# Optimization experiments

Measured on AMD Instinct MI355X. Metric: run time of the kernel, lower is better.

The kernel has to match this reference:

```python
import jax, jax.numpy as jnp
import numpy as np
from jax import lax

DN = ('NHWC', 'HWIO', 'NHWC')
COMMIT = 0.25  # commitment_cost


def _conv(x, w, b, s):
    return lax.conv_general_dilated(x, w, (s, s), 'SAME', dimension_numbers=DN) + b


def _convT(x, w, b, s):
    return lax.conv_transpose(x, w, (s, s), 'SAME', dimension_numbers=DN) + b


def setup_inputs() -> dict:
    key = jax.random.key(0)
    ks = jax.random.split(key, 12)
    B, H, W = 128, 128, 128
    D, K = 64, 512  # embedding_dim, num_embeddings

    def wp(k, shape):
        fan_in = shape[0] * shape[1] * shape[2]
        return (jax.random.normal(k, shape, jnp.float32) / np.sqrt(fan_in)).astype(jnp.float32)

    return {
        'x': jax.random.uniform(ks[0], (B, H, W, 3), jnp.float32),
        'enc_w1': wp(ks[1], (4, 4, 3, 32)),   'enc_b1': jnp.zeros((32,), jnp.float32),
        'enc_w2': wp(ks[2], (4, 4, 32, 64)),  'enc_b2': jnp.zeros((64,), jnp.float32),
        'enc_w3': wp(ks[3], (4, 4, 64, 128)), 'enc_b3': jnp.zeros((128,), jnp.float32),
        'enc_w4': wp(ks[4], (2, 2, 128, D)),  'enc_b4': jnp.zeros((D,), jnp.float32),
        'emb': jax.random.normal(ks[5], (K, D), jnp.float32),
        'dec_w1': wp(ks[6], (2, 2, D, 128)),  'dec_b1': jnp.zeros((128,), jnp.float32),
        'dec_w2': wp(ks[7], (4, 4, 128, 64)), 'dec_b2': jnp.zeros((64,), jnp.float32),
        'dec_w3': wp(ks[8], (4, 4, 64, 32)),  'dec_b3': jnp.zeros((32,), jnp.float32),
        'dec_w4': wp(ks[9], (4, 4, 32, 3)),   'dec_b4': jnp.zeros((3,), jnp.float32),
    }


def _forward(x, enc_w1, enc_b1, enc_w2, enc_b2, enc_w3, enc_b3, enc_w4, enc_b4,
             emb, dec_w1, dec_b1, dec_w2, dec_b2, dec_w3, dec_b3, dec_w4, dec_b4):
    # ---- encoder: 128 -> 64 -> 32 -> 16 (SAME, stride 2) -> 16 (stride 1) ----
    z = jax.nn.relu(_conv(x, enc_w1, enc_b1, 2))
    z = jax.nn.relu(_conv(z, enc_w2, enc_b2, 2))
    z = jax.nn.relu(_conv(z, enc_w3, enc_b3, 2))
    z = _conv(z, enc_w4, enc_b4, 1)                     # [B, 16, 16, D]

    # ---- vector quantizer ----
    B, D = z.shape[0], emb.shape[1]
    flat = z.reshape(B, -1, D)                          # [B, N, D]
    d2 = (jnp.sum(flat * flat, axis=2, keepdims=True)
          - 2.0 * jnp.einsum('bnd,kd->bnk', flat, emb)
          + jnp.sum(emb * emb, axis=1))                 # [B, N, K]
    idx = jnp.argmin(d2, axis=2)                        # [B, N] int
    q = emb[idx].reshape(z.shape)                       # gather == one_hot @ emb
    loss = COMMIT * jnp.mean((lax.stop_gradient(q) - z) ** 2)
    q_st = z + lax.stop_gradient(q - z)                 # straight-through

    # ---- decoder: 16 -> 16 (stride 1) -> 32 -> 64 -> 128 ----
    y = jax.nn.relu(_convT(q_st, dec_w1, dec_b1, 1))
    y = jax.nn.relu(_convT(y, dec_w2, dec_b2, 2))
    y = jax.nn.relu(_convT(y, dec_w3, dec_b3, 2))
    y = jax.nn.sigmoid(_convT(y, dec_w4, dec_b4, 2))    # [B, 128, 128, 3]
    return y, loss, idx


def reference(x, enc_w1, enc_b1, enc_w2, enc_b2, enc_w3, enc_b3, enc_w4, enc_b4,
              emb, dec_w1, dec_b1, dec_w2, dec_b2, dec_w3, dec_b3, dec_w4, dec_b4):
    return _forward(x, enc_w1, enc_b1, enc_w2, enc_b2, enc_w3, enc_b3, enc_w4, enc_b4,
                    emb, dec_w1, dec_b1, dec_w2, dec_b2, dec_w3, dec_b3, dec_w4, dec_b4)
```

## Files before the change

kernel.cpp:

```cpp
#include <hip/hip_runtime.h>
#include <hip/hip_bf16.h>

typedef __bf16 bf16x8_t __attribute__((ext_vector_type(8)));
typedef float  f32x4_t  __attribute__((ext_vector_type(4)));

__device__ inline bf16x8_t ld_bf16x8(const __hip_bfloat16* p) {
    return *reinterpret_cast<const bf16x8_t*>(p);
}
__device__ inline bf16x8_t zero_bf16x8() {
    bf16x8_t z;
#pragma unroll
    for (int i = 0; i < 8; ++i) z[i] = (__bf16)0.0f;
    return z;
}

__device__ inline void split3f(float v, __bf16& h, __bf16& m, __bf16& l) {
    unsigned u;  __builtin_memcpy(&u, &v, 4);
    unsigned uh = u & 0xffff0000u;
    float fh;    __builtin_memcpy(&fh, &uh, 4);
    float r = v - fh;
    unsigned ur; __builtin_memcpy(&ur, &r, 4);
    unsigned um = ur & 0xffff0000u;
    float fm;    __builtin_memcpy(&fm, &um, 4);
    float r2 = r - fm;
    unsigned ul; __builtin_memcpy(&ul, &r2, 4);
    unsigned short hs = (unsigned short)(uh >> 16);
    unsigned short ms = (unsigned short)(um >> 16);
    unsigned short ls = (unsigned short)(ul >> 16);
    __builtin_memcpy(&h, &hs, 2);
    __builtin_memcpy(&m, &ms, 2);
    __builtin_memcpy(&l, &ls, 2);
}

__global__ __launch_bounds__(256) void enc1_kernel(
    const float* __restrict__ x, const float* __restrict__ w,
    const float* __restrict__ bias, float* __restrict__ y)
{
    __shared__ float xs[34*66*3];
    __shared__ float wsm[1536];

    const int n  = blockIdx.x >> 3;
    const int th = (blockIdx.x >> 1) & 3;
    const int tw = blockIdx.x & 1;
    const int HO0 = th*16, WO0 = tw*32;
    const int HI0 = 2*HO0 - 1, WI0 = 2*WO0 - 1;
    const int t = threadIdx.x;

    for (int i = t; i < 1536; i += 256) wsm[i] = w[i];
    for (int i = t; i < 34*66*3; i += 256) {
        int row = i / 198; int j = i - row*198;
        int wi_l = j / 3;  int c = j - wi_l*3;
        int hi = HI0 + row, wi = WI0 + wi_l;
        float v = 0.0f;
        if (hi >= 0 && hi < 128 && wi >= 0 && wi < 128)
            v = x[((n*128 + hi)*128 + wi)*3 + c];
        xs[i] = v;
    }
    __syncthreads();

    const int wl = t & 15, hl = t >> 4;
    float acc0[32], acc1[32];
#pragma unroll
    for (int f4 = 0; f4 < 8; ++f4) {
        float4 bv = *(const float4*)(bias + 4*f4);
        acc0[4*f4+0]=bv.x; acc0[4*f4+1]=bv.y; acc0[4*f4+2]=bv.z; acc0[4*f4+3]=bv.w;
        acc1[4*f4+0]=bv.x; acc1[4*f4+1]=bv.y; acc1[4*f4+2]=bv.z; acc1[4*f4+3]=bv.w;
    }
    for (int r = 0; r < 4; ++r) {
#pragma unroll
        for (int s = 0; s < 4; ++s) {
#pragma unroll
            for (int c = 0; c < 3; ++c) {
                float xv0 = xs[(2*hl + r)*198 + (2*wl + s)*3 + c];
                float xv1 = xs[(2*hl + r)*198 + (2*(wl+16) + s)*3 + c];
                const float* wp = wsm + ((r*4 + s)*3 + c)*32;
#pragma unroll
                for (int f4 = 0; f4 < 8; ++f4) {
                    float4 wv = *(const float4*)(wp + 4*f4);
                    acc0[4*f4+0] = fmaf(xv0, wv.x, acc0[4*f4+0]);
                    acc0[4*f4+1] = fmaf(xv0, wv.y, acc0[4*f4+1]);
                    acc0[4*f4+2] = fmaf(xv0, wv.z, acc0[4*f4+2]);
                    acc0[4*f4+3] = fmaf(xv0, wv.w, acc0[4*f4+3]);
                    acc1[4*f4+0] = fmaf(xv1, wv.x, acc1[4*f4+0]);
                    acc1[4*f4+1] = fmaf(xv1, wv.y, acc1[4*f4+1]);
                    acc1[4*f4+2] = fmaf(xv1, wv.z, acc1[4*f4+2]);
                    acc1[4*f4+3] = fmaf(xv1, wv.w, acc1[4*f4+3]);
                }
            }
        }
    }
    float* y0 = y + ((size_t)((n*64 + HO0 + hl)*64) + WO0 + wl)*32;
#pragma unroll
    for (int f4 = 0; f4 < 8; ++f4) {
        float4 o0 = make_float4(fmaxf(acc0[4*f4+0],0.f), fmaxf(acc0[4*f4+1],0.f),
                                fmaxf(acc0[4*f4+2],0.f), fmaxf(acc0[4*f4+3],0.f));
        *(float4*)(y0 + 4*f4) = o0;
    }
    float* y1 = y0 + 16*32;
#pragma unroll
    for (int f4 = 0; f4 < 8; ++f4) {
        float4 o1 = make_float4(fmaxf(acc1[4*f4+0],0.f), fmaxf(acc1[4*f4+1],0.f),
                                fmaxf(acc1[4*f4+2],0.f), fmaxf(acc1[4*f4+3],0.f));
        *(float4*)(y1 + 4*f4) = o1;
    }
}

__global__ void prep_wpk(const float* __restrict__ w, __hip_bfloat16* __restrict__ out,
                         int TAPS, int CIN, int COUT)
{
    const int NF = COUT >> 4, KC = CIN >> 5;
    int total = TAPS*3*NF*KC*512;
    int i = blockIdx.x*256 + threadIdx.x;
    if (i >= total) return;
    int tmp = i;
    int j = tmp & 7;      tmp >>= 3;
    int lane = tmp & 63;  tmp >>= 6;
    int kc = tmp % KC;    tmp /= KC;
    int nf = tmp % NF;    tmp /= NF;
    int plane = tmp % 3;  int tap = tmp / 3;
    int l15 = lane & 15, quad = lane >> 4;
    int f = nf*16 + l15;
    int c = kc*32 + quad*8 + j;
    float v = w[(tap*CIN + c)*COUT + f];
    __bf16 h, m, l;
    split3f(v, h, m, l);
    ((__bf16*)out)[i] = (plane == 0) ? h : (plane == 1) ? m : l;
}

__global__ void prep_wdk(const float* __restrict__ w, __hip_bfloat16* __restrict__ out,
                         int TAPS, int CIN, int COUT)
{
    const int NF = COUT >> 4, KC = CIN >> 5;
    int total = TAPS*NF*KC*512;
    int i = blockIdx.x*256 + threadIdx.x;
    if (i >= total) return;
    int tmp = i;
    int j = tmp & 7;      tmp >>= 3;
    int lane = tmp & 63;  tmp >>= 6;
    int kc = tmp % KC;    tmp /= KC;
    int nf = tmp % NF;    tmp /= NF;
    int tap = tmp;
    int l15 = lane & 15, quad = lane >> 4;
    int f = nf*16 + l15;
    int c = kc*32 + quad*8 + j;
    out[i] = __float2bfloat16(w[(tap*CIN + c)*COUT + f]);
}

__global__ void prep_wb4(const float* __restrict__ w, __hip_bfloat16* __restrict__ out)
{
    int i = blockIdx.x*256 + threadIdx.x;
    if (i >= 16*64*8) return;
    int j = i & 7;
    int lane = (i >> 3) & 63;
    int g = i >> 9;
    int f = lane & 15;
    int c = (lane >> 4)*8 + j;
    float v = (f < 3) ? w[g*96 + c*3 + f] : 0.0f;
    out[i] = __float2bfloat16(v);
}

__global__ void prep_wek(const float* __restrict__ emb, __hip_bfloat16* __restrict__ out)
{
    int i = blockIdx.x*256 + threadIdx.x;
    if (i >= 32*2*3*512) return;
    int tmp = i;
    int j = tmp & 7;      tmp >>= 3;
    int lane = tmp & 63;  tmp >>= 6;
    int plane = tmp % 3;  tmp /= 3;
    int kc = tmp & 1;     int nf = tmp >> 1;
    int code = nf*16 + (lane & 15);
    int c = kc*32 + (lane >> 4)*8 + j;
    float v = emb[code*64 + c];
    __bf16 h, m, l;
    split3f(v, h, m, l);
    ((__bf16*)out)[i] = (plane == 0) ? h : (plane == 1) ? m : l;
}

__global__ void prep_se(const float* __restrict__ emb, float* __restrict__ se)
{
    int k = blockIdx.x*256 + threadIdx.x;
    if (k >= 512) return;
    float s = 0.0f;
    for (int d = 0; d < 64; ++d) {
        float e = emb[k*64 + d];
        s = fmaf(e, e, s);
    }
    se[k] = s;
}

template<int R,int S,int CIN,int COUT,int IWL,int OWL,int STR,int PAD,int ACT,int INF32,int OUTF32,int NSPLIT>
__global__ __launch_bounds__(256) void mfma_encB(
    const void* __restrict__ xin,
    const __hip_bfloat16* __restrict__ wpk,
    const float* __restrict__ bias,
    __hip_bfloat16* __restrict__ yout,
    float* __restrict__ yf)
{
    constexpr int IW = 1 << IWL, OW = 1 << OWL;
    constexpr int NF = COUT / 16, KC = CIN / 32, TAPS = R*S;
    constexpr int NFB = NF / NSPLIT;
    constexpr int PIECE = NFB*KC*64;
    constexpr int CHUNK8 = 3*PIECE;
    __shared__ bf16x8_t ldsB[CHUNK8];

    const int nf0 = (int)blockIdx.y * NFB;
    const int t = threadIdx.x;
    const int wave = t >> 6, lane = t & 63;
    const int l15 = lane & 15, quad = lane >> 4;

    const int m  = blockIdx.x*64 + wave*16 + l15;
    const int wp_ = m & (OW-1);
    const int hp_ = (m >> OWL) & (OW-1);
    const int np_ = m >> (2*OWL);

    f32x4_t acc[NFB];
#pragma unroll
    for (int nf = 0; nf < NFB; ++nf) {
        float bv = bias[(nf0 + nf)*16 + l15];
        acc[nf][0] = bv; acc[nf][1] = bv; acc[nf][2] = bv; acc[nf][3] = bv;
    }
    const bf16x8_t zv = zero_bf16x8();

    for (int tap = 0; tap < TAPS; ++tap) {
        __syncthreads();
        {
            const bf16x8_t* base = (const bf16x8_t*)wpk + (size_t)tap*(3*NF*KC*64);
            for (int i8 = t; i8 < CHUNK8; i8 += 256) {
                int plane = i8 / PIECE;
                int rem = i8 - plane*PIECE;
                ldsB[i8] = base[(size_t)(plane*NF + nf0)*KC*64 + rem];
            }
        }
        __syncthreads();

        const int r = tap / S, s = tap % S;
        const int hi = hp_*STR - PAD + r;
        const int wi = wp_*STR - PAD + s;
        const bool v = (hi >= 0) && (hi < IW) && (wi >= 0) && (wi < IW);
        const int hic = v ? hi : 0, wic = v ? wi : 0;
        const size_t pix = (size_t)(np_*IW + hic)*IW + wic;

#pragma unroll
        for (int kc = 0; kc < KC; ++kc) {
            bf16x8_t ah, am_, al_;
            if (INF32) {
                const float* af = (const float*)xin + pix*CIN + kc*32 + quad*8;
                float xv[8];
                if (v) {
                    *(float4*)(xv+0) = *(const float4*)(af);
                    *(float4*)(xv+4) = *(const float4*)(af + 4);
                } else {
#pragma unroll
                    for (int jj = 0; jj < 8; ++jj) xv[jj] = 0.0f;
                }
#pragma unroll
                for (int jj = 0; jj < 8; ++jj) {
                    __bf16 th, tm, tl;
                    split3f(xv[jj], th, tm, tl);
                    ah[jj] = th; am_[jj] = tm; al_[jj] = tl;
                }
            } else {
                const __hip_bfloat16* ap = (const __hip_bfloat16*)xin
                    + pix*(3*CIN) + kc*32 + quad*8;
                ah  = v ? ld_bf16x8(ap)           : zv;
                am_ = v ? ld_bf16x8(ap + CIN)     : zv;
                al_ = v ? ld_bf16x8(ap + 2*CIN)   : zv;
            }
#pragma unroll
            for (int nf = 0; nf < NFB; ++nf) {
                bf16x8_t bh = ldsB[(0*NFB + nf)*KC*64 + kc*64 + lane];
                bf16x8_t bm = ldsB[(1*NFB + nf)*KC*64 + kc*64 + lane];
                bf16x8_t bl = ldsB[(2*NFB + nf)*KC*64 + kc*64 + lane];
                acc[nf] = __builtin_amdgcn_mfma_f32_16x16x32_bf16(al_, bh, acc[nf], 0, 0, 0);
                acc[nf] = __builtin_amdgcn_mfma_f32_16x16x32_bf16(ah,  bl, acc[nf], 0, 0, 0);
                acc[nf] = __builtin_amdgcn_mfma_f32_16x16x32_bf16(am_, bm, acc[nf], 0, 0, 0);
                acc[nf] = __builtin_amdgcn_mfma_f32_16x16x32_bf16(am_, bh, acc[nf], 0, 0, 0);
                acc[nf] = __builtin_amdgcn_mfma_f32_16x16x32_bf16(ah,  bm, acc[nf], 0, 0, 0);
                acc[nf] = __builtin_amdgcn_mfma_f32_16x16x32_bf16(ah,  bh, acc[nf], 0, 0, 0);
            }
        }
    }

#pragma unroll
    for (int nf = 0; nf < NFB; ++nf) {
#pragma unroll
        for (int i = 0; i < 4; ++i) {
            int mo = blockIdx.x*64 + wave*16 + quad*4 + i;
            int wo = mo & (OW-1), ho = (mo >> OWL) & (OW-1), no = mo >> (2*OWL);
            size_t opix = (size_t)(no*OW + ho)*OW + wo;
            float vv = acc[nf][i];
            if (ACT) vv = fmaxf(vv, 0.0f);
            if (OUTF32) {
                yf[opix*COUT + (nf0 + nf)*16 + l15] = vv;
            } else {
                __bf16 h, mm2, l;
                split3f(vv, h, mm2, l);
                __bf16* yb = (__bf16*)yout + opix*(3*COUT) + (nf0 + nf)*16 + l15;
                yb[0]        = h;
                yb[COUT]     = mm2;
                yb[2*COUT]   = l;
            }
        }
    }
}

template<int CIN,int COUT,int SWL,int CONVT,int NSPLIT>
__global__ __launch_bounds__(256) void mfma_decB(
    const __hip_bfloat16* __restrict__ xin,
    const __hip_bfloat16* __restrict__ wdk,
    const float* __restrict__ bias,
    __hip_bfloat16* __restrict__ yout)
{
    constexpr int SW = 1 << SWL;
    constexpr int NF = COUT / 16, KC = CIN / 32;
    constexpr int NFB = NF / NSPLIT;
    constexpr int CHUNK8 = NFB*KC*64;
    __shared__ bf16x8_t ldsB[CHUNK8];

    const int ph = CONVT ? (int)(blockIdx.y >> 1) : 0;
    const int pw = CONVT ? (int)(blockIdx.y & 1) : 0;
    const int nf0 = (CONVT ? (int)blockIdx.z : (int)blockIdx.y) * NFB;
    const int t = threadIdx.x;
    const int wave = t >> 6, lane = t & 63;
    const int l15 = lane & 15, quad = lane >> 4;

    const int m  = blockIdx.x*64 + wave*16 + l15;
    const int wp_ = m & (SW-1);
    const int hp_ = (m >> SWL) & (SW-1);
    const int np_ = m >> (2*SWL);

    f32x4_t acc[NFB];
#pragma unroll
    for (int nf = 0; nf < NFB; ++nf) {
        float bv = bias[(nf0 + nf)*16 + l15];
        acc[nf][0] = bv; acc[nf][1] = bv; acc[nf][2] = bv; acc[nf][3] = bv;
    }
    const bf16x8_t zv = zero_bf16x8();

    for (int tap = 0; tap < 4; ++tap) {
        const int rr = tap >> 1, ss = tap & 1;
        const int widx = CONVT ? ((ph + 2*rr)*4 + (pw + 2*ss)) : tap;
        __syncthreads();
        {
            const bf16x8_t* base = (const bf16x8_t*)wdk
                + (size_t)widx*(NF*KC*64) + (size_t)nf0*KC*64;
            for (int i8 = t; i8 < CHUNK8; i8 += 256) ldsB[i8] = base[i8];
        }
        __syncthreads();

        const int hi = hp_ + ph - 1 + rr;
        const int wi = wp_ + pw - 1 + ss;
        const bool v = (hi >= 0) && (hi < SW) && (wi >= 0) && (wi < SW);
        const int hic = v ? hi : 0, wic = v ? wi : 0;
        const __hip_bfloat16* ap = xin + (size_t)((np_*SW + hic)*SW + wic)*CIN + quad*8;
#pragma unroll
        for (int kc = 0; kc < KC; ++kc) {
            bf16x8_t a = v ? ld_bf16x8(ap + kc*32) : zv;
#pragma unroll
            for (int nf = 0; nf < NFB; ++nf) {
                bf16x8_t b = ldsB[(nf*KC + kc)*64 + lane];
                acc[nf] = __builtin_amdgcn_mfma_f32_16x16x32_bf16(a, b, acc[nf], 0, 0, 0);
            }
        }
    }

    constexpr int HOUT = CONVT ? 2*SW : SW;
#pragma unroll
    for (int nf = 0; nf < NFB; ++nf) {
#pragma unroll
        for (int i = 0; i < 4; ++i) {
            int mo = blockIdx.x*64 + wave*16 + quad*4 + i;
            int wo = mo & (SW-1), ho = (mo >> SWL) & (SW-1), no = mo >> (2*SWL);
            int hoo = CONVT ? 2*ho + ph : ho;
            int woo = CONVT ? 2*wo + pw : wo;
            float vv = fmaxf(acc[nf][i], 0.0f);
            yout[((size_t)(no*HOUT + hoo)*HOUT + woo)*COUT + (nf0 + nf)*16 + l15] = __float2bfloat16(vv);
        }
    }
}

__global__ __launch_bounds__(256) void dec4_mfma(
    const __hip_bfloat16* __restrict__ x, const __hip_bfloat16* __restrict__ wb,
    const float* __restrict__ bias, float* __restrict__ y)
{
    __shared__ __hip_bfloat16 xs[6*66*40];

    const int n  = blockIdx.x >> 4;
    const int R0 = (blockIdx.x & 15) * 4;
    const int t  = threadIdx.x;
    const int wave = t >> 6, lane = t & 63;
    const int l15 = lane & 15, quad = lane >> 4;

    bf16x8_t wreg[16];
#pragma unroll
    for (int g = 0; g < 16; ++g)
        wreg[g] = ld_bf16x8(wb + (size_t)(g*64 + lane)*8);

    const float bv = (l15 < 3) ? bias[l15] : 0.0f;

    for (int slot = t; slot < 6*66*4; slot += 256) {
        int row = slot / 264;
        int rem = slot - row*264;
        int col = rem >> 2, c8 = rem & 3;
        int xi = R0 - 1 + row, xc = col - 1;
        uint4 val = make_uint4(0u,0u,0u,0u);
        if (xi >= 0 && xi < 64 && xc >= 0 && xc < 64)
            val = *(const uint4*)(x + ((size_t)((n*64 + xi)*64) + xc)*32 + c8*8);
        *(uint4*)(xs + (row*66 + col)*40 + c8*8) = val;
    }
    __syncthreads();

    for (int r4 = 0; r4 < 4; ++r4) {
        bf16x8_t af[3][3];
#pragma unroll
        for (int dr = 0; dr < 3; ++dr)
#pragma unroll
            for (int dc = 0; dc < 3; ++dc)
                af[dr][dc] = *(const bf16x8_t*)(xs
                    + ((r4 + dr)*66 + (wave*16 + l15 + dc))*40 + quad*8);

#pragma unroll
        for (int ph = 0; ph < 2; ++ph)
#pragma unroll
        for (int pw = 0; pw < 2; ++pw) {
            f32x4_t acc;
            acc[0] = bv; acc[1] = bv; acc[2] = bv; acc[3] = bv;
#pragma unroll
            for (int rr = 0; rr < 2; ++rr)
#pragma unroll
            for (int ss = 0; ss < 2; ++ss) {
                const int g = (ph + 2*rr)*4 + (pw + 2*ss);
                acc = __builtin_amdgcn_mfma_f32_16x16x32_bf16(
                          af[ph+rr][pw+ss], wreg[g], acc, 0, 0, 0);
            }
            if (l15 < 3) {
#pragma unroll
                for (int i = 0; i < 4; ++i) {
                    int pc = wave*16 + quad*4 + i;
                    int ho = 2*(R0 + r4) + ph, wo = 2*pc + pw;
                    float vv = 1.0f / (1.0f + __expf(-acc[i]));
                    y[((size_t)(n*128 + ho)*128 + wo)*3 + l15] = vv;
                }
            }
        }
    }
}

__global__ void zero_loss(float* p) {
    if (threadIdx.x == 0 && blockIdx.x == 0) *p = 0.0f;
}

__global__ __launch_bounds__(256) void vq_mfma(
    const float* __restrict__ z, const __hip_bfloat16* __restrict__ wek,
    const float* __restrict__ se, const float* __restrict__ emb,
    __hip_bfloat16* __restrict__ qb, float* __restrict__ idx_out,
    float* __restrict__ loss_out, float loss_scale)
{
    __shared__ float ses[512];
    __shared__ float rv[64*16];
    __shared__ int   ri[64*16];
    __shared__ int   mi[64];
    __shared__ float lred[256];

    const int t = threadIdx.x;
    const int wave = t >> 6, lane = t & 63;
    const int l15 = lane & 15, quad = lane >> 4;
    const int pos0 = blockIdx.x * 64;

    for (int i = t; i < 512; i += 256) ses[i] = se[i];

    const int prow = pos0 + wave*16 + l15;
    bf16x8_t ah[2], am[2], al[2];
#pragma unroll
    for (int kc = 0; kc < 2; ++kc) {
        float xv[8];
        *(float4*)(xv+0) = *(const float4*)(z + (size_t)prow*64 + kc*32 + quad*8);
        *(float4*)(xv+4) = *(const float4*)(z + (size_t)prow*64 + kc*32 + quad*8 + 4);
#pragma unroll
        for (int jj = 0; jj < 8; ++jj) {
            __bf16 th, tm, tl;
            split3f(xv[jj], th, tm, tl);
            ah[kc][jj] = th; am[kc][jj] = tm; al[kc][jj] = tl;
        }
    }

    f32x4_t acc[32];
#pragma unroll
    for (int nf = 0; nf < 32; ++nf) {
        acc[nf][0] = 0.f; acc[nf][1] = 0.f; acc[nf][2] = 0.f; acc[nf][3] = 0.f;
    }

#pragma unroll 8
    for (int nf = 0; nf < 32; ++nf) {
#pragma unroll
        for (int kc = 0; kc < 2; ++kc) {
            const bf16x8_t* bp = (const bf16x8_t*)wek + (size_t)((nf*2 + kc)*3)*64 + lane;
            bf16x8_t bh = bp[0];
            bf16x8_t bm = bp[64];
            bf16x8_t bl = bp[128];
            acc[nf] = __builtin_amdgcn_mfma_f32_16x16x32_bf16(al[kc], bh, acc[nf], 0, 0, 0);
            acc[nf] = __builtin_amdgcn_mfma_f32_16x16x32_bf16(ah[kc], bl, acc[nf], 0, 0, 0);
            acc[nf] = __builtin_amdgcn_mfma_f32_16x16x32_bf16(am[kc], bm, acc[nf], 0, 0, 0);
            acc[nf] = __builtin_amdgcn_mfma_f32_16x16x32_bf16(am[kc], bh, acc[nf], 0, 0, 0);
            acc[nf] = __builtin_amdgcn_mfma_f32_16x16x32_bf16(ah[kc], bm, acc[nf], 0, 0, 0);
            acc[nf] = __builtin_amdgcn_mfma_f32_16x16x32_bf16(ah[kc], bh, acc[nf], 0, 0, 0);
        }
    }
    __syncthreads();

    float best[4]; int bidx[4];
#pragma unroll
    for (int i = 0; i < 4; ++i) { best[i] = 3.4e38f; bidx[i] = 0; }
#pragma unroll
    for (int nf = 0; nf < 32; ++nf) {
        const int code = nf*16 + l15;
        const float seC = ses[code];
#pragma unroll
        for (int i = 0; i < 4; ++i) {
            float d = fmaf(-2.0f, acc[nf][i], seC);
            if (d < best[i]) { best[i] = d; bidx[i] = code; }
        }
    }
#pragma unroll
    for (int i = 0; i < 4; ++i) {
        int p = wave*16 + quad*4 + i;
        rv[p*16 + l15] = best[i];
        ri[p*16 + l15] = bidx[i];
    }
    __syncthreads();
    if (t < 64) {
        float bd = rv[t*16]; int bi = ri[t*16];
#pragma unroll
        for (int k = 1; k < 16; ++k) {
            float v = rv[t*16 + k]; int id = ri[t*16 + k];
            if (v < bd || (v == bd && id < bi)) { bd = v; bi = id; }
        }
        mi[t] = bi;
        idx_out[pos0 + t] = (float)bi;
    }
    __syncthreads();

    float part = 0.0f;
    for (int j = t; j < 4096; j += 256) {
        int p = j >> 6, d = j & 63;
        float ev = emb[(size_t)mi[p]*64 + d];
        float zz = z[(size_t)(pos0 + p)*64 + d];
        float df = ev - zz;
        part = fmaf(df, df, part);
        qb[(size_t)pos0*64 + j] = __float2bfloat16(ev);
    }
    lred[t] = part;
    __syncthreads();
    for (int s = 128; s > 0; s >>= 1) {
        if (t < s) lred[t] += lred[t + s];
        __syncthreads();
    }
    if (t == 0) atomicAdd(loss_out, lred[0] * loss_scale);
}

extern "C" void kernel_launch(void* const* d_in, const int* in_sizes, int n_in,
                              void* d_out, int out_size, void* d_ws, size_t ws_size,
                              hipStream_t stream)
{
    const float* x   = (const float*)d_in[0];
    const float* ew1 = (const float*)d_in[1];  const float* eb1 = (const float*)d_in[2];
    const float* ew2 = (const float*)d_in[3];  const float* eb2 = (const float*)d_in[4];
    const float* ew3 = (const float*)d_in[5];  const float* eb3 = (const float*)d_in[6];
    const float* ew4 = (const float*)d_in[7];  const float* eb4 = (const float*)d_in[8];
    const float* emb = (const float*)d_in[9];
    const float* dw1 = (const float*)d_in[10]; const float* db1 = (const float*)d_in[11];
    const float* dw2 = (const float*)d_in[12]; const float* db2 = (const float*)d_in[13];
    const float* dw3 = (const float*)d_in[14]; const float* db3 = (const float*)d_in[15];
    const float* dw4 = (const float*)d_in[16]; const float* db4 = (const float*)d_in[17];

    float* outy = (float*)d_out;
    float* outl = outy + 6291456;
    float* outi = outl + 1;

    char* W = (char*)d_ws;
    float*          e1  = (float*)         (W + 0);
    __hip_bfloat16* e2p = (__hip_bfloat16*)(W + 67108864);
    __hip_bfloat16* e3p = (__hip_bfloat16*)(W + 0);
    float*          z   = (float*)         (W + 25165824);
    __hip_bfloat16* qb  = (__hip_bfloat16*)(W + 33554432);
    __hip_bfloat16* d1o = (__hip_bfloat16*)(W + 37748736);
    __hip_bfloat16* d2o = (__hip_bfloat16*)(W + 46137344);
    __hip_bfloat16* d3o = (__hip_bfloat16*)(W + 67108864);
    __hip_bfloat16* wp2 = (__hip_bfloat16*)(W + 117440512);
    __hip_bfloat16* wp3 = wp2 + 98304;
    __hip_bfloat16* wp4 = wp3 + 393216;
    __hip_bfloat16* wd1 = wp4 + 98304;
    __hip_bfloat16* wd2 = wd1 + 32768;
    __hip_bfloat16* wd3 = wd2 + 131072;
    __hip_bfloat16* wb4 = wd3 + 32768;
    __hip_bfloat16* wek = wb4 + 8192;
    float*          seb = (float*)(wek + 98304);

    hipLaunchKernelGGL(prep_wpk, dim3(384),  dim3(256), 0, stream, ew2, wp2, 16, 32, 64);
    hipLaunchKernelGGL(prep_wpk, dim3(1536), dim3(256), 0, stream, ew3, wp3, 16, 64, 128);
    hipLaunchKernelGGL(prep_wpk, dim3(384),  dim3(256), 0, stream, ew4, wp4, 4, 128, 64);
    hipLaunchKernelGGL(prep_wdk, dim3(128),  dim3(256), 0, stream, dw1, wd1, 4, 64, 128);
    hipLaunchKernelGGL(prep_wdk, dim3(512),  dim3(256), 0, stream, dw2, wd2, 16, 128, 64);
    hipLaunchKernelGGL(prep_wdk, dim3(128),  dim3(256), 0, stream, dw3, wd3, 16, 64, 32);
    hipLaunchKernelGGL(prep_wb4, dim3(32),   dim3(256), 0, stream, dw4, wb4);
    hipLaunchKernelGGL(prep_wek, dim3(384),  dim3(256), 0, stream, emb, wek);
    hipLaunchKernelGGL(prep_se,  dim3(2),    dim3(256), 0, stream, emb, seb);

    hipLaunchKernelGGL(enc1_kernel, dim3(1024), dim3(256), 0, stream, x, ew1, eb1, e1);
    hipLaunchKernelGGL((mfma_encB<4,4,32,64,6,5,2,1,1,1,0,1>), dim3(2048), dim3(256), 0, stream,
                       (const void*)e1, wp2, eb2, e2p, (float*)nullptr);
    hipLaunchKernelGGL((mfma_encB<4,4,64,128,5,4,2,1,1,0,0,2>), dim3(512,2), dim3(256), 0, stream,
                       (const void*)e2p, wp3, eb3, e3p, (float*)nullptr);
    hipLaunchKernelGGL((mfma_encB<2,2,128,64,4,4,1,0,0,0,1,2>), dim3(512,2), dim3(256), 0, stream,
                       (const void*)e3p, wp4, eb4, (__hip_bfloat16*)nullptr, z);

    hipLaunchKernelGGL(zero_loss, dim3(1), dim3(64), 0, stream, outl);
    hipLaunchKernelGGL(vq_mfma, dim3(512), dim3(256), 0, stream,
                       z, wek, seb, emb, qb, outi, outl, 0.25f / 2097152.0f);

    hipLaunchKernelGGL((mfma_decB<64,128,4,0,2>), dim3(512,2),  dim3(256), 0, stream, qb,  wd1, db1, d1o);
    hipLaunchKernelGGL((mfma_decB<128,64,4,1,1>), dim3(512,4),  dim3(256), 0, stream, d1o, wd2, db2, d2o);
    hipLaunchKernelGGL((mfma_decB<64,32,5,1,1>),  dim3(2048,4), dim3(256), 0, stream, d2o, wd3, db3, d3o);
    hipLaunchKernelGGL(dec4_mfma, dim3(2048), dim3(256), 0, stream, d3o, wb4, db4, outy);
}
```

Measured before the change: 535.5 us.

## Move first encoder conv to bf16x3-split MFMA and retile enc3 grid

New measurement: 548.4 us. 2.4% more time.

```diff
diff --git a/kernel.cpp b/kernel.cpp
--- a/kernel.cpp
+++ b/kernel.cpp
@@ -32,77 +32,98 @@
     __builtin_memcpy(&l, &ls, 2);
 }
 
-__global__ __launch_bounds__(256) void enc1_kernel(
-    const float* __restrict__ x, const float* __restrict__ w,
+__global__ __launch_bounds__(256) void enc1_mfma(
+    const float* __restrict__ x,
+    const __hip_bfloat16* __restrict__ wb,
     const float* __restrict__ bias, float* __restrict__ y)
 {
-    __shared__ float xs[34*66*3];
-    __shared__ float wsm[1536];
-
-    const int n  = blockIdx.x >> 3;
-    const int th = (blockIdx.x >> 1) & 3;
-    const int tw = blockIdx.x & 1;
-    const int HO0 = th*16, WO0 = tw*32;
-    const int HI0 = 2*HO0 - 1, WI0 = 2*WO0 - 1;
-    const int t = threadIdx.x;
-
-    for (int i = t; i < 1536; i += 256) wsm[i] = w[i];
-    for (int i = t; i < 34*66*3; i += 256) {
-        int row = i / 198; int j = i - row*198;
-        int wi_l = j / 3;  int c = j - wi_l*3;
-        int hi = HI0 + row, wi = WI0 + wi_l;
+    __shared__ bf16x8_t xs8[1584];
+    __hip_bfloat16* xs = (__hip_bfloat16*)xs8;
+
+    const int n  = blockIdx.x >> 6;
+    const int ho = blockIdx.x & 63;
+    const int t  = threadIdx.x;
+    const int wave = t >> 6, lane = t & 63;
+    const int l15 = lane & 15, quad = lane >> 4;
+
+    bf16x8_t bf[2][2][3];
+#pragma unroll
+    for (int rp = 0; rp < 2; ++rp)
+#pragma unroll
+        for (int tile = 0; tile < 2; ++tile)
+#pragma unroll
+            for (int pl = 0; pl < 3; ++pl)
+                bf[rp][tile][pl] = ld_bf16x8(wb + (size_t)((((rp*2 + tile)*3 + pl)*64 + lane))*8);
+
+    const int hi0 = 2*ho - 1;
+    for (int slot = t; slot < 4*132*4; slot += 256) {
+        int row = slot / 528;
+        int rem = slot - row*528;
+        int col = rem >> 2, c = rem & 3;
+        int hi = hi0 + row, wi = col - 1;
         float v = 0.0f;
-        if (hi >= 0 && hi < 128 && wi >= 0 && wi < 128)
-            v = x[((n*128 + hi)*128 + wi)*3 + c];
-        xs[i] = v;
+        if (c < 3 && hi >= 0 && hi < 128 && wi >= 0 && wi < 128)
+            v = x[((size_t)((n*128 + hi))*128 + wi)*3 + c];
+        __bf16 h, m, l;
+        split3f(v, h, m, l);
+        xs[0*2112 + slot] = *(__hip_bfloat16*)&h;
+        xs[1*2112 + slot] = *(__hip_bfloat16*)&m;
+        xs[2*2112 + slot] = *(__hip_bfloat16*)&l;
     }
     __syncthreads();
 
-    const int wl = t & 15, hl = t >> 4;
-    float acc0[32], acc1[32];
-#pragma unroll
-    for (int f4 = 0; f4 < 8; ++f4) {
-        float4 bv = *(const float4*)(bias + 4*f4);
-        acc0[4*f4+0]=bv.x; acc0[4*f4+1]=bv.y; acc0[4*f4+2]=bv.z; acc0[4*f4+3]=bv.w;
-        acc1[4*f4+0]=bv.x; acc1[4*f4+1]=bv.y; acc1[4*f4+2]=bv.z; acc1[4*f4+3]=bv.w;
-    }
-    for (int r = 0; r < 4; ++r) {
-#pragma unroll
-        for (int s = 0; s < 4; ++s) {
-#pragma unroll
-            for (int c = 0; c < 3; ++c) {
-                float xv0 = xs[(2*hl + r)*198 + (2*wl + s)*3 + c];
-                float xv1 = xs[(2*hl + r)*198 + (2*(wl+16) + s)*3 + c];
-                const float* wp = wsm + ((r*4 + s)*3 + c)*32;
-#pragma unroll
-                for (int f4 = 0; f4 < 8; ++f4) {
-                    float4 wv = *(const float4*)(wp + 4*f4);
-                    acc0[4*f4+0] = fmaf(xv0, wv.x, acc0[4*f4+0]);
-                    acc0[4*f4+1] = fmaf(xv0, wv.y, acc0[4*f4+1]);
-                    acc0[4*f4+2] = fmaf(xv0, wv.z, acc0[4*f4+2]);
-                    acc0[4*f4+3] = fmaf(xv0, wv.w, acc0[4*f4+3]);
-                    acc1[4*f4+0] = fmaf(xv1, wv.x, acc1[4*f4+0]);
-                    acc1[4*f4+1] = fmaf(xv1, wv.y, acc1[4*f4+1]);
-                    acc1[4*f4+2] = fmaf(xv1, wv.z, acc1[4*f4+2]);
-                    acc1[4*f4+3] = fmaf(xv1, wv.w, acc1[4*f4+3]);
-                }
-            }
-        }
-    }
-    float* y0 = y + ((size_t)((n*64 + HO0 + hl)*64) + WO0 + wl)*32;
-#pragma unroll
-    for (int f4 = 0; f4 < 8; ++f4) {
-        float4 o0 = make_float4(fmaxf(acc0[4*f4+0],0.f), fmaxf(acc0[4*f4+1],0.f),
-                                fmaxf(acc0[4*f4+2],0.f), fmaxf(acc0[4*f4+3],0.f));
-        *(float4*)(y0 + 4*f4) = o0;
-    }
-    float* y1 = y0 + 16*32;
-#pragma unroll
-    for (int f4 = 0; f4 < 8; ++f4) {
-        float4 o1 = make_float4(fmaxf(acc1[4*f4+0],0.f), fmaxf(acc1[4*f4+1],0.f),
-                                fmaxf(acc1[4*f4+2],0.f), fmaxf(acc1[4*f4+3],0.f));
-        *(float4*)(y1 + 4*f4) = o1;
-    }
+    const int wo = wave*16 + l15;
+    f32x4_t acc[2];
+#pragma unroll
+    for (int tile = 0; tile < 2; ++tile) {
+        float bv = bias[tile*16 + l15];
+        acc[tile][0] = bv; acc[tile][1] = bv; acc[tile][2] = bv; acc[tile][3] = bv;
+    }
+
+#pragma unroll
+    for (int rp = 0; rp < 2; ++rp) {
+        const int off = (2*rp + (quad >> 1))*528 + 8*wo + (quad & 1)*8;
+        bf16x8_t ah = *(const bf16x8_t*)(xs + 0*2112 + off);
+        bf16x8_t am = *(const bf16x8_t*)(xs + 1*2112 + off);
+        bf16x8_t al = *(const bf16x8_t*)(xs + 2*2112 + off);
+#pragma unroll
+        for (int tile = 0; tile < 2; ++tile) {
+            acc[tile] = __builtin_amdgcn_mfma_f32_16x16x32_bf16(al, bf[rp][tile][0], acc[tile], 0, 0, 0);
+            acc[tile] = __builtin_amdgcn_mfma_f32_16x16x32_bf16(ah, bf[rp][tile][2], acc[tile], 0, 0, 0);
+            acc[tile] = __builtin_amdgcn_mfma_f32_16x16x32_bf16(am, bf[rp][tile][1], acc[tile], 0, 0, 0);
+            acc[tile] = __builtin_amdgcn_mfma_f32_16x16x32_bf16(am, bf[rp][tile][0], acc[tile], 0, 0, 0);
+            acc[tile] = __builtin_amdgcn_mfma_f32_16x16x32_bf16(ah, bf[rp][tile][1], acc[tile], 0, 0, 0);
+            acc[tile] = __builtin_amdgcn_mfma_f32_16x16x32_bf16(ah, bf[rp][tile][0], acc[tile], 0, 0, 0);
+        }
+    }
+
+#pragma unroll
+    for (int tile = 0; tile < 2; ++tile)
+#pragma unroll
+        for (int i = 0; i < 4; ++i) {
+            int wo2 = wave*16 + quad*4 + i;
+            float vv = fmaxf(acc[tile][i], 0.0f);
+            y[((size_t)((n*64 + ho))*64 + wo2)*32 + tile*16 + l15] = vv;
+        }
+}
+
+__global__ void prep_wb1(const float* __restrict__ w, __hip_bfloat16* __restrict__ out)
+{
+    int i = blockIdx.x*256 + threadIdx.x;
+    if (i >= 2*2*3*64*8) return;
+    int j = i & 7;
+    int lane = (i >> 3) & 63;
+    int g = i >> 9;
+    int pl = g % 3; g /= 3;
+    int tile = g & 1, rp = g >> 1;
+    int k = (lane >> 4)*8 + j;
+    int c = k & 3, s = (k >> 2) & 3, lr = k >> 4;
+    int f = tile*16 + (lane & 15);
+    float v = 0.0f;
+    if (c < 3) v = w[(((rp*2 + lr)*4 + s)*3 + c)*32 + f];
+    __bf16 h, m, l;
+    split3f(v, h, m, l);
+    ((__bf16*)out)[i] = (pl == 0) ? h : (pl == 1) ? m : l;
 }
 
 __global__ void prep_wpk(const float* __restrict__ w, __hip_bfloat16* __restrict__ out,
@@ -595,6 +616,7 @@
     __hip_bfloat16* wb4 = wd3 + 32768;
     __hip_bfloat16* wek = wb4 + 8192;
     float*          seb = (float*)(wek + 98304);
+    __hip_bfloat16* wb1 = (__hip_bfloat16*)(seb + 512);
 
     hipLaunchKernelGGL(prep_wpk, dim3(384),  dim3(256), 0, stream, ew2, wp2, 16, 32, 64);
     hipLaunchKernelGGL(prep_wpk, dim3(1536), dim3(256), 0, stream, ew3, wp3, 16, 64, 128);
@@ -605,11 +627,12 @@
     hipLaunchKernelGGL(prep_wb4, dim3(32),   dim3(256), 0, stream, dw4, wb4);
     hipLaunchKernelGGL(prep_wek, dim3(384),  dim3(256), 0, stream, emb, wek);
     hipLaunchKernelGGL(prep_se,  dim3(2),    dim3(256), 0, stream, emb, seb);
-
-    hipLaunchKernelGGL(enc1_kernel, dim3(1024), dim3(256), 0, stream, x, ew1, eb1, e1);
+    hipLaunchKernelGGL(prep_wb1, dim3(24),   dim3(256), 0, stream, ew1, wb1);
+
+    hipLaunchKernelGGL(enc1_mfma, dim3(8192), dim3(256), 0, stream, x, wb1, eb1, e1);
     hipLaunchKernelGGL((mfma_encB<4,4,32,64,6,5,2,1,1,1,0,1>), dim3(2048), dim3(256), 0, stream,
                        (const void*)e1, wp2, eb2, e2p, (float*)nullptr);
-    hipLaunchKernelGGL((mfma_encB<4,4,64,128,5,4,2,1,1,0,0,2>), dim3(512,2), dim3(256), 0, stream,
+    hipLaunchKernelGGL((mfma_encB<4,4,64,128,5,4,2,1,1,0,0,4>), dim3(512,4), dim3(256), 0, stream,
                        (const void*)e2p, wp3, eb3, e3p, (float*)nullptr);
     hipLaunchKernelGGL((mfma_encB<2,2,128,64,4,4,1,0,0,0,1,2>), dim3(512,2), dim3(256), 0, stream,
                        (const void*)e3p, wp4, eb4, (__hip_bfloat16*)nullptr, z);
```
